# Kernel tuning notes

Measured on AMD Instinct MI355X. Metric: run time of the kernel, lower is better.

The kernel has to match this reference:

```python
import jax, jax.numpy as jnp
import numpy as np

N_NODES = 50000
N_EDGES = 800000
DIM = 64
BN_EPS = 1e-5


def setup_inputs() -> dict:
    key = jax.random.key(0)
    ks = jax.random.split(key, 9)
    s = 1.0 / np.sqrt(DIM)
    feature = jax.random.normal(ks[0], (N_NODES, DIM), jnp.float32)
    edge_index = jax.random.randint(ks[1], (2, N_EDGES), 0, N_NODES)
    Wk = jax.random.normal(ks[2], (DIM, DIM), jnp.float32) * s
    Wq = jax.random.normal(ks[3], (DIM, DIM), jnp.float32) * s
    Wv = jax.random.normal(ks[4], (DIM, DIM), jnp.float32) * s
    bk = jax.random.normal(ks[5], (DIM,), jnp.float32) * 0.01
    bq = jax.random.normal(ks[6], (DIM,), jnp.float32) * 0.01
    bv = jax.random.normal(ks[7], (DIM,), jnp.float32) * 0.01
    bias = jax.random.normal(ks[8], (DIM,), jnp.float32) * 0.01
    gamma = jnp.ones((DIM,), jnp.float32)
    beta = jnp.zeros((DIM,), jnp.float32)
    return dict(feature=feature, edge_index=edge_index, Wk=Wk, bk=bk,
                Wq=Wq, bq=bq, Wv=Wv, bv=bv, bias=bias, gamma=gamma, beta=beta)


def reference(feature, edge_index, Wk, bk, Wq, bq, Wv, bv, bias, gamma, beta):
    # Node-level projections (dense GEMMs on [N, D])
    K = feature @ Wk + bk   # applied to x_i (dst)
    Q = feature @ Wq + bq   # applied to x_j (src)
    V = feature @ Wv + bv   # applied to x_j (src)
    src, dst = edge_index[0], edge_index[1]
    # Per-edge gather -> sigmoid gate -> gated message  [E, D]
    eta = jax.nn.sigmoid(K[dst] + Q[src])
    msg = eta * V[src]
    # Scatter-add into destination nodes  [N, D]
    agg = jax.ops.segment_sum(msg, dst, num_segments=feature.shape[0])
    h = agg + bias
    # BatchNorm1d over nodes (batch statistics, biased variance) + ReLU
    mean = jnp.mean(h, axis=0)
    var = jnp.var(h, axis=0)
    h = (h - mean) * jax.lax.rsqrt(var + BN_EPS) * gamma + beta
    return jax.nn.relu(h)
```

## Files before the change

### kernel.cpp

```cpp
#include <hip/hip_runtime.h>
#include <hip/hip_fp16.h>
#include <stdint.h>

#define N_NODES 50000
#define N_EDGES 800000
#define DIM 64
#define BN_EPS 1e-5f
#define CAP 64
#define ZERO_NODE N_NODES
#define POISON 0xAAAAAAAAu

#define NPTILES 391
#define FUSED_BLOCKS 1173

#define NBINS 241
#define BIN_W 208
#define BINCAP 4352

#define NTILES 3125
#define NSTATS_REP 8

typedef _Float16 f16;
typedef __attribute__((ext_vector_type(8))) _Float16 f16x8;
typedef __attribute__((ext_vector_type(4))) float f32x4;

#define LPITCH 72

__global__ __launch_bounds__(256, 4) void proj_bin_kernel(
    const float* __restrict__ feat,
    const float* __restrict__ Wk, const float* __restrict__ Wq,
    const float* __restrict__ Wv,
    const float* __restrict__ bk, const float* __restrict__ bq,
    const float* __restrict__ bv,
    __half* __restrict__ Kh, __half* __restrict__ QV,
    const int* __restrict__ ei, uint32_t* __restrict__ binCursor,
    uint32_t* __restrict__ binArr)
{
  __shared__ f16 sWt[DIM][LPITCH];
  __shared__ uint32_t hist[NBINS];
  __shared__ uint32_t gbase[NBINS];

  const int b = blockIdx.x;
  const int tid = threadIdx.x;
  const int m3 = b % 3;

  if (m3 != 0) {
    const int sid = (b / 3) * 2 + (m3 - 1);
    const int e0 = sid * 1024;
    const int e1 = (e0 + 1024 < N_EDGES) ? e0 + 1024 : N_EDGES;
    if (tid < NBINS) hist[tid] = 0;
    __syncthreads();

    int n = 0; int bn[4]; uint32_t pk[4], rk[4];
    const int base = e0 + tid * 4;
    if (base + 4 <= e1) {
      const int4 s4 = *(const int4*)(ei + base);
      const int4 d4 = *(const int4*)(ei + N_EDGES + base);
      const int ss[4] = {s4.x, s4.y, s4.z, s4.w};
      const int dd[4] = {d4.x, d4.y, d4.z, d4.w};
#pragma unroll
      for (int j = 0; j < 4; ++j) {
        const int bin = dd[j] / BIN_W;
        bn[j] = bin;
        pk[j] = (uint32_t)ss[j] | ((uint32_t)(dd[j] - bin * BIN_W) << 16);
        rk[j] = atomicAdd(&hist[bin], 1u);
      }
      n = 4;
    } else {
      for (int e = base; e < e1; ++e) {
        const int src = ei[e];
        const int dst = ei[N_EDGES + e];
        const int bin = dst / BIN_W;
        bn[n] = bin;
        pk[n] = (uint32_t)src | ((uint32_t)(dst - bin * BIN_W) << 16);
        rk[n] = atomicAdd(&hist[bin], 1u);
        ++n;
      }
    }
    __syncthreads();
    if (tid < NBINS)
      gbase[tid] = hist[tid] ? (atomicAdd(&binCursor[tid * 16], hist[tid])
                                - POISON) : 0u;
    __syncthreads();
    for (int j = 0; j < n; ++j) {
      const uint32_t pos = gbase[bn[j]] + rk[j];
      if (pos < BINCAP) binArr[(uint32_t)bn[j] * BINCAP + pos] = pk[j];
    }
    return;
  }

  const int tile0 = (b / 3) * 128;
  const int lane = tid & 63;
  const int w = tid >> 6;
  const int nl = lane & 15;
  const int kg = lane >> 4;

  f16x8 fb[2][2];
#pragma unroll
  for (int g2 = 0; g2 < 2; ++g2) {
    const int node = tile0 + w * 32 + g2 * 16 + nl;
    const bool ok = node < N_NODES;
    const float* fp = feat + (size_t)(ok ? node : 0) * DIM;
#pragma unroll
    for (int kk = 0; kk < 2; ++kk) {
      const float4 x0 = ((const float4*)(fp + kk * 32 + kg * 8))[0];
      const float4 x1 = ((const float4*)(fp + kk * 32 + kg * 8))[1];
      f16x8 r;
      r[0] = (f16)x0.x; r[1] = (f16)x0.y; r[2] = (f16)x0.z; r[3] = (f16)x0.w;
      r[4] = (f16)x1.x; r[5] = (f16)x1.y; r[6] = (f16)x1.z; r[7] = (f16)x1.w;
      if (!ok) r = (f16x8)(f16)0.f;
      fb[g2][kk] = r;
    }
  }

#pragma unroll
  for (int m = 0; m < 3; ++m) {
    const float* __restrict__ Wm = (m == 0) ? Wk : (m == 1) ? Wq : Wv;
    const float* __restrict__ bb = (m == 0) ? bk : (m == 1) ? bq : bv;

    __syncthreads();
    for (int i = tid; i < 1024; i += 256) {
      const int c = i & 63;
      const int kq = i >> 6;
      union { f16 h[4]; uint2 u; } pkw;
      pkw.h[0] = (f16)Wm[(kq * 4 + 0) * 64 + c];
      pkw.h[1] = (f16)Wm[(kq * 4 + 1) * 64 + c];
      pkw.h[2] = (f16)Wm[(kq * 4 + 2) * 64 + c];
      pkw.h[3] = (f16)Wm[(kq * 4 + 3) * 64 + c];
      *(uint2*)&sWt[c][kq * 4] = pkw.u;
    }
    __syncthreads();

    f16x8 fa[4][2];
#pragma unroll
    for (int nt = 0; nt < 4; ++nt)
#pragma unroll
      for (int kk = 0; kk < 2; ++kk)
        fa[nt][kk] = *(const f16x8*)&sWt[nt * 16 + nl][kk * 32 + kg * 8];
    f32x4 bias[4];
#pragma unroll
    for (int nt = 0; nt < 4; ++nt)
      bias[nt] = *(const f32x4*)&bb[nt * 16 + kg * 4];

#pragma unroll
    for (int g2 = 0; g2 < 2; ++g2) {
      const int node = tile0 + w * 32 + g2 * 16 + nl;
      f32x4 acc[4];
#pragma unroll
      for (int nt = 0; nt < 4; ++nt) acc[nt] = bias[nt];
#pragma unroll
      for (int kk = 0; kk < 2; ++kk)
#pragma unroll
        for (int nt = 0; nt < 4; ++nt)
          acc[nt] = __builtin_amdgcn_mfma_f32_16x16x32_f16(
              fa[nt][kk], fb[g2][kk], acc[nt], 0, 0, 0);

      if (m == 0) {
        if (node < N_NODES) {
#pragma unroll
          for (int nt = 0; nt < 4; ++nt) {
            union { __half2 h[2]; uint2 u; } pkk;
            pkk.h[0] = __floats2half2_rn(acc[nt][0], acc[nt][1]);
            pkk.h[1] = __floats2half2_rn(acc[nt][2], acc[nt][3]);
            ((uint2*)Kh)[node * 16 + nt * 4 + kg] = pkk.u;
          }
        }
      } else {
        if (node <= N_NODES) {
          const int half = (m == 1) ? 0 : 1;
#pragma unroll
          for (int nt = 0; nt < 4; ++nt) {
            union { __half2 h[2]; uint2 u; } pkk;
            pkk.h[0] = __floats2half2_rn(acc[nt][0], acc[nt][1]);
            pkk.h[1] = __floats2half2_rn(acc[nt][2], acc[nt][3]);
            if (node == N_NODES) { pkk.u.x = 0u; pkk.u.y = 0u; }
            ((uint2*)QV)[node * 32 + (nt * 4 + kg) * 2 + half] = pkk.u;
          }
        }
      }
    }
  }
}

__device__ __forceinline__ float4 edge_acc(float4 acc, const float4 k,
                                           const uint4 qv)
{
  union { uint32_t u; __half2 h; } q0, q1, v0, v1;
  q0.u = qv.x; q1.u = qv.y; v0.u = qv.z; v1.u = qv.w;
  const float2 qa = __half22float2(q0.h);
  const float2 qb = __half22float2(q1.h);
  const float2 va = __half22float2(v0.h);
  const float2 vb = __half22float2(v1.h);
  acc.x += va.x * __builtin_amdgcn_rcpf(1.0f + __expf(-(k.x + qa.x)));
  acc.y += va.y * __builtin_amdgcn_rcpf(1.0f + __expf(-(k.y + qa.y)));
  acc.z += vb.x * __builtin_amdgcn_rcpf(1.0f + __expf(-(k.z + qb.x)));
  acc.w += vb.y * __builtin_amdgcn_rcpf(1.0f + __expf(-(k.w + qb.y)));
  return acc;
}

__global__ __launch_bounds__(256) void aggregate_kernel(
    const uint32_t* __restrict__ binArr, const uint32_t* __restrict__ binCursor,
    const uint2* __restrict__ Kh2, const uint4* __restrict__ QV4,
    float4* __restrict__ agg4, float* __restrict__ stats)
{
  __shared__ uint16_t slist[16][CAP];
  __shared__ uint32_t lcnt[16];
  const int tid = threadIdx.x;
  const int tile = blockIdx.x;
  const int g = tile / 13;
  const uint32_t lo = (uint32_t)((tile - g * 13) * 16);

  if (tid < 16) lcnt[tid] = 0;
  __syncthreads();

  uint32_t cnt = binCursor[g * 16] - POISON;
  if (cnt > BINCAP) cnt = BINCAP;
  const uint32_t* arr = binArr + (uint32_t)g * BINCAP;

  for (uint32_t i = tid * 4; i < cnt; i += 1024) {
    if (i + 4 <= cnt) {
      const uint4 p4 = *(const uint4*)(arr + i);
      const uint32_t ps[4] = {p4.x, p4.y, p4.z, p4.w};
#pragma unroll
      for (int j = 0; j < 4; ++j) {
        const uint32_t idx = (ps[j] >> 16) - lo;
        if (idx < 16u) {
          const uint32_t r = atomicAdd(&lcnt[idx], 1u);
          if (r < CAP) slist[idx][r] = (uint16_t)(ps[j] & 0xFFFFu);
        }
      }
    } else {
      for (uint32_t e = i; e < cnt; ++e) {
        const uint32_t p = arr[e];
        const uint32_t idx = (p >> 16) - lo;
        if (idx < 16u) {
          const uint32_t r = atomicAdd(&lcnt[idx], 1u);
          if (r < CAP) slist[idx][r] = (uint16_t)(p & 0xFFFFu);
        }
      }
    }
  }
  __syncthreads();

  const int row = tid >> 4;
  const int t = tid & 15;
  const int n = tile * 16 + row;

  union { uint2 u; __half2 h[2]; } kun;
  kun.u = Kh2[n * 16 + t];
  const float2 k0 = __half22float2(kun.h[0]);
  const float2 k1 = __half22float2(kun.h[1]);
  const float4 k = make_float4(k0.x, k0.y, k1.x, k1.y);

  int deg = (int)lcnt[row];
  if (deg > CAP) deg = CAP;
  float4 acc = make_float4(0.f, 0.f, 0.f, 0.f);

  for (int j0 = 0; j0 < deg; j0 += 16) {
    const int navail = deg - j0;
    const int s = (t < navail) ? (int)slist[row][j0 + t] : ZERO_NODE;

    int sA[8]; uint4 qvA[8];
#pragma unroll
    for (int i = 0; i < 8; ++i) sA[i] = __shfl(s, i, 16);
#pragma unroll
    for (int i = 0; i < 8; ++i) qvA[i] = QV4[sA[i] * 16 + t];

    const bool haveB = navail > 8;
    int sB[8]; uint4 qvB[8];
    if (haveB) {
#pragma unroll
      for (int i = 0; i < 8; ++i) sB[i] = __shfl(s, 8 + i, 16);
#pragma unroll
      for (int i = 0; i < 8; ++i) qvB[i] = QV4[sB[i] * 16 + t];
    }

#pragma unroll
    for (int i = 0; i < 8; ++i) acc = edge_acc(acc, k, qvA[i]);
    if (haveB) {
#pragma unroll
      for (int i = 0; i < 8; ++i) acc = edge_acc(acc, k, qvB[i]);
    }
  }
  agg4[n * 16 + t] = acc;

  __shared__ float sred[2][16][DIM + 4];
  float4 pssq;
  pssq.x = acc.x * acc.x; pssq.y = acc.y * acc.y;
  pssq.z = acc.z * acc.z; pssq.w = acc.w * acc.w;
  *(float4*)&sred[0][row][t * 4] = acc;
  *(float4*)&sred[1][row][t * 4] = pssq;
  __syncthreads();
  if (tid < 128) {
    const int s = tid >> 6, c = tid & 63;
    float v = 0.0f;
#pragma unroll
    for (int r = 0; r < 16; ++r) v += sred[s][r][c];
    atomicAdd(&stats[(blockIdx.x & (NSTATS_REP - 1)) * 128 + tid], v);
  }
}

__global__ __launch_bounds__(256) void out_kernel(
    float* __restrict__ out, const float* __restrict__ stats,
    const float* __restrict__ gamma, const float* __restrict__ beta)
{
  __shared__ float sstats[128];
  const int tid = threadIdx.x;
  if (tid < 128) {
    float v = 0.0f;
#pragma unroll
    for (int r = 0; r < NSTATS_REP; ++r) v += stats[r * 128 + tid];
    sstats[tid] = v;
  }
  __syncthreads();

  const int idx = blockIdx.x * 256 + tid;
  if (idx >= N_NODES * (DIM / 4)) return;
  const int t = idx & 15;
  const float4 v = ((const float4*)out)[idx];
  const float invN = 1.0f / (float)N_NODES;
  const float vin[4] = { v.x, v.y, v.z, v.w };
  float o[4];
#pragma unroll
  for (int j = 0; j < 4; ++j) {
    const int c = t * 4 + j;
    const float mean = sstats[c] * invN;
    float var = sstats[DIM + c] * invN - mean * mean;
    var = var < 0.0f ? 0.0f : var;
    const float scale = rsqrtf(var + BN_EPS) * gamma[c];
    const float shift = beta[c] - mean * scale;
    const float x = vin[j] * scale + shift;
    o[j] = x > 0.0f ? x : 0.0f;
  }
  float4 r; r.x = o[0]; r.y = o[1]; r.z = o[2]; r.w = o[3];
  ((float4*)out)[idx] = r;
}

extern "C" void kernel_launch(void* const* d_in, const int* in_sizes, int n_in,
                              void* d_out, int out_size, void* d_ws, size_t ws_size,
                              hipStream_t stream) {
  (void)in_sizes; (void)n_in; (void)out_size; (void)ws_size;
  const float* feat  = (const float*)d_in[0];
  const int*   ei    = (const int*)d_in[1];
  const float* Wk    = (const float*)d_in[2];
  const float* bk    = (const float*)d_in[3];
  const float* Wq    = (const float*)d_in[4];
  const float* bq    = (const float*)d_in[5];
  const float* Wv    = (const float*)d_in[6];
  const float* bv    = (const float*)d_in[7];
  const float* gamma = (const float*)d_in[9];
  const float* beta  = (const float*)d_in[10];

  char* base = (char*)d_ws;
  __half*   Kh       = (__half*)base;
  __half*   QV       = (__half*)(base + 6400000);
  float*    stats    = (float*)(base + 19200256);
  uint32_t* binCursor= (uint32_t*)(base + 19204352);
  uint32_t* binArr   = (uint32_t*)(base + 19219776);

  proj_bin_kernel<<<FUSED_BLOCKS, 256, 0, stream>>>(
      feat, Wk, Wq, Wv, bk, bq, bv, Kh, QV, ei, binCursor, binArr);

  aggregate_kernel<<<NTILES, 256, 0, stream>>>(
      binArr, binCursor, (const uint2*)Kh, (const uint4*)QV, (float4*)d_out,
      stats);

  out_kernel<<<(N_NODES * (DIM / 4) + 255) / 256, 256, 0, stream>>>(
      (float*)d_out, stats, gamma, beta);
}
```

Before: 160.3 us.

## Process two 16-node tiles per aggregate block with XCD-aware block remapping

```diff
diff --git a/kernel.cpp b/kernel.cpp
--- a/kernel.cpp
+++ b/kernel.cpp
@@ -13,11 +13,12 @@
 #define NPTILES 391
 #define FUSED_BLOCKS 1173
 
-#define NBINS 241
-#define BIN_W 208
-#define BINCAP 4352
+#define NBINS 224
+#define BIN_W 224
+#define BINCAP 4608
 
 #define NTILES 3125
+#define AGG_BLOCKS 1563
 #define NSTATS_REP 8
 
 typedef _Float16 f16;
@@ -203,14 +204,19 @@
     const uint2* __restrict__ Kh2, const uint4* __restrict__ QV4,
     float4* __restrict__ agg4, float* __restrict__ stats)
 {
-  __shared__ uint16_t slist[16][CAP];
-  __shared__ uint32_t lcnt[16];
+  __shared__ uint16_t slist[32][CAP];
+  __shared__ uint32_t lcnt[32];
   const int tid = threadIdx.x;
-  const int tile = blockIdx.x;
-  const int g = tile / 13;
-  const uint32_t lo = (uint32_t)((tile - g * 13) * 16);
-
-  if (tid < 16) lcnt[tid] = 0;
+
+  const int bid = blockIdx.x;
+  const int xcd = bid % 8;
+  const int start = (xcd < 3) ? xcd * 196 : 3 * 196 + (xcd - 3) * 195;
+  const int w = start + bid / 8;
+
+  const int g = w / 7;
+  const uint32_t lo = (uint32_t)((w - g * 7) * 32);
+
+  if (tid < 32) lcnt[tid] = 0;
   __syncthreads();
 
   uint32_t cnt = binCursor[g * 16] - POISON;
@@ -224,7 +230,7 @@
 #pragma unroll
       for (int j = 0; j < 4; ++j) {
         const uint32_t idx = (ps[j] >> 16) - lo;
-        if (idx < 16u) {
+        if (idx < 32u) {
           const uint32_t r = atomicAdd(&lcnt[idx], 1u);
           if (r < CAP) slist[idx][r] = (uint16_t)(ps[j] & 0xFFFFu);
         }
@@ -233,7 +239,7 @@
       for (uint32_t e = i; e < cnt; ++e) {
         const uint32_t p = arr[e];
         const uint32_t idx = (p >> 16) - lo;
-        if (idx < 16u) {
+        if (idx < 32u) {
           const uint32_t r = atomicAdd(&lcnt[idx], 1u);
           if (r < CAP) slist[idx][r] = (uint16_t)(p & 0xFFFFu);
         }
@@ -244,51 +250,60 @@
 
   const int row = tid >> 4;
   const int t = tid & 15;
-  const int n = tile * 16 + row;
-
-  union { uint2 u; __half2 h[2]; } kun;
-  kun.u = Kh2[n * 16 + t];
-  const float2 k0 = __half22float2(kun.h[0]);
-  const float2 k1 = __half22float2(kun.h[1]);
-  const float4 k = make_float4(k0.x, k0.y, k1.x, k1.y);
-
-  int deg = (int)lcnt[row];
-  if (deg > CAP) deg = CAP;
-  float4 acc = make_float4(0.f, 0.f, 0.f, 0.f);
-
-  for (int j0 = 0; j0 < deg; j0 += 16) {
-    const int navail = deg - j0;
-    const int s = (t < navail) ? (int)slist[row][j0 + t] : ZERO_NODE;
-
-    int sA[8]; uint4 qvA[8];
-#pragma unroll
-    for (int i = 0; i < 8; ++i) sA[i] = __shfl(s, i, 16);
-#pragma unroll
-    for (int i = 0; i < 8; ++i) qvA[i] = QV4[sA[i] * 16 + t];
-
-    const bool haveB = navail > 8;
-    int sB[8]; uint4 qvB[8];
-    if (haveB) {
-#pragma unroll
-      for (int i = 0; i < 8; ++i) sB[i] = __shfl(s, 8 + i, 16);
-#pragma unroll
-      for (int i = 0; i < 8; ++i) qvB[i] = QV4[sB[i] * 16 + t];
-    }
-
-#pragma unroll
-    for (int i = 0; i < 8; ++i) acc = edge_acc(acc, k, qvA[i]);
-    if (haveB) {
-#pragma unroll
-      for (int i = 0; i < 8; ++i) acc = edge_acc(acc, k, qvB[i]);
-    }
-  }
-  agg4[n * 16 + t] = acc;
+  float4 psum = make_float4(0.f, 0.f, 0.f, 0.f);
+  float4 pssq = make_float4(0.f, 0.f, 0.f, 0.f);
+
+#pragma unroll
+  for (int pass = 0; pass < 2; ++pass) {
+    const int tile = w * 2 + pass;
+    if (tile >= NTILES) break;
+    const int lrow = pass * 16 + row;
+    const int n = tile * 16 + row;
+
+    union { uint2 u; __half2 h[2]; } kun;
+    kun.u = Kh2[n * 16 + t];
+    const float2 k0 = __half22float2(kun.h[0]);
+    const float2 k1 = __half22float2(kun.h[1]);
+    const float4 k = make_float4(k0.x, k0.y, k1.x, k1.y);
+
+    int deg = (int)lcnt[lrow];
+    if (deg > CAP) deg = CAP;
+    float4 acc = make_float4(0.f, 0.f, 0.f, 0.f);
+
+    for (int j0 = 0; j0 < deg; j0 += 16) {
+      const int navail = deg - j0;
+      const int s = (t < navail) ? (int)slist[lrow][j0 + t] : ZERO_NODE;
+
+      int sA[8]; uint4 qvA[8];
+#pragma unroll
+      for (int i = 0; i < 8; ++i) sA[i] = __shfl(s, i, 16);
+#pragma unroll
+      for (int i = 0; i < 8; ++i) qvA[i] = QV4[sA[i] * 16 + t];
+
+      const bool haveB = navail > 8;
+      int sB[8]; uint4 qvB[8];
+      if (haveB) {
+#pragma unroll
+        for (int i = 0; i < 8; ++i) sB[i] = __shfl(s, 8 + i, 16);
+#pragma unroll
+        for (int i = 0; i < 8; ++i) qvB[i] = QV4[sB[i] * 16 + t];
+      }
+
+#pragma unroll
+      for (int i = 0; i < 8; ++i) acc = edge_acc(acc, k, qvA[i]);
+      if (haveB) {
+#pragma unroll
+        for (int i = 0; i < 8; ++i) acc = edge_acc(acc, k, qvB[i]);
+      }
+    }
+    agg4[n * 16 + t] = acc;
+    psum.x += acc.x; psum.y += acc.y; psum.z += acc.z; psum.w += acc.w;
+    pssq.x += acc.x * acc.x; pssq.y += acc.y * acc.y;
+    pssq.z += acc.z * acc.z; pssq.w += acc.w * acc.w;
+  }
 
   __shared__ float sred[2][16][DIM + 4];
-  float4 pssq;
-  pssq.x = acc.x * acc.x; pssq.y = acc.y * acc.y;
-  pssq.z = acc.z * acc.z; pssq.w = acc.w * acc.w;
-  *(float4*)&sred[0][row][t * 4] = acc;
+  *(float4*)&sred[0][row][t * 4] = psum;
   *(float4*)&sred[1][row][t * 4] = pssq;
   __syncthreads();
   if (tid < 128) {
@@ -296,7 +311,7 @@
     float v = 0.0f;
 #pragma unroll
     for (int r = 0; r < 16; ++r) v += sred[s][r][c];
-    atomicAdd(&stats[(blockIdx.x & (NSTATS_REP - 1)) * 128 + tid], v);
+    atomicAdd(&stats[(bid & (NSTATS_REP - 1)) * 128 + tid], v);
   }
 }
 
@@ -356,12 +371,12 @@
   __half*   QV       = (__half*)(base + 6400000);
   float*    stats    = (float*)(base + 19200256);
   uint32_t* binCursor= (uint32_t*)(base + 19204352);
-  uint32_t* binArr   = (uint32_t*)(base + 19219776);
+  uint32_t* binArr   = (uint32_t*)(base + 19218688);
 
   proj_bin_kernel<<<FUSED_BLOCKS, 256, 0, stream>>>(
       feat, Wk, Wq, Wv, bk, bq, bv, Kh, QV, ei, binCursor, binArr);
 
-  aggregate_kernel<<<NTILES, 256, 0, stream>>>(
+  aggregate_kernel<<<AGG_BLOCKS, 256, 0, stream>>>(
       binArr, binCursor, (const uint2*)Kh, (const uint4*)QV, (float4*)d_out,
       stats);
 
```

After: 153.3 us (median of 2 runs). 4.4% less time.

## Remap aggregate tiles per XCD, widen bins, preload all weights once

Applied to the files above, without the earlier changes.

```diff
diff --git a/kernel.cpp b/kernel.cpp
--- a/kernel.cpp
+++ b/kernel.cpp
@@ -13,9 +13,9 @@
 #define NPTILES 391
 #define FUSED_BLOCKS 1173
 
-#define NBINS 241
-#define BIN_W 208
-#define BINCAP 4352
+#define NBINS 224
+#define BIN_W 224
+#define BINCAP 4608
 
 #define NTILES 3125
 #define NSTATS_REP 8
@@ -36,7 +36,7 @@
     const int* __restrict__ ei, uint32_t* __restrict__ binCursor,
     uint32_t* __restrict__ binArr)
 {
-  __shared__ f16 sWt[DIM][LPITCH];
+  __shared__ f16 sWt[3][DIM][LPITCH];
   __shared__ uint32_t hist[NBINS];
   __shared__ uint32_t gbase[NBINS];
 
@@ -95,6 +95,20 @@
   const int nl = lane & 15;
   const int kg = lane >> 4;
 
+  for (int i = tid; i < 3 * 1024; i += 256) {
+    const int m = i >> 10;
+    const int rem = i & 1023;
+    const int c = rem & 63;
+    const int kq = rem >> 6;
+    const float* __restrict__ W = (m == 0) ? Wk : (m == 1) ? Wq : Wv;
+    union { f16 h[4]; uint2 u; } pkw;
+    pkw.h[0] = (f16)W[(kq * 4 + 0) * 64 + c];
+    pkw.h[1] = (f16)W[(kq * 4 + 1) * 64 + c];
+    pkw.h[2] = (f16)W[(kq * 4 + 2) * 64 + c];
+    pkw.h[3] = (f16)W[(kq * 4 + 3) * 64 + c];
+    *(uint2*)&sWt[m][c][kq * 4] = pkw.u;
+  }
+
   f16x8 fb[2][2];
 #pragma unroll
   for (int g2 = 0; g2 < 2; ++g2) {
@@ -112,31 +126,18 @@
       fb[g2][kk] = r;
     }
   }
+  __syncthreads();
 
 #pragma unroll
   for (int m = 0; m < 3; ++m) {
-    const float* __restrict__ Wm = (m == 0) ? Wk : (m == 1) ? Wq : Wv;
     const float* __restrict__ bb = (m == 0) ? bk : (m == 1) ? bq : bv;
 
-    __syncthreads();
-    for (int i = tid; i < 1024; i += 256) {
-      const int c = i & 63;
-      const int kq = i >> 6;
-      union { f16 h[4]; uint2 u; } pkw;
-      pkw.h[0] = (f16)Wm[(kq * 4 + 0) * 64 + c];
-      pkw.h[1] = (f16)Wm[(kq * 4 + 1) * 64 + c];
-      pkw.h[2] = (f16)Wm[(kq * 4 + 2) * 64 + c];
-      pkw.h[3] = (f16)Wm[(kq * 4 + 3) * 64 + c];
-      *(uint2*)&sWt[c][kq * 4] = pkw.u;
-    }
-    __syncthreads();
-
     f16x8 fa[4][2];
 #pragma unroll
     for (int nt = 0; nt < 4; ++nt)
 #pragma unroll
       for (int kk = 0; kk < 2; ++kk)
-        fa[nt][kk] = *(const f16x8*)&sWt[nt * 16 + nl][kk * 32 + kg * 8];
+        fa[nt][kk] = *(const f16x8*)&sWt[m][nt * 16 + nl][kk * 32 + kg * 8];
     f32x4 bias[4];
 #pragma unroll
     for (int nt = 0; nt < 4; ++nt)
@@ -206,9 +207,14 @@
   __shared__ uint16_t slist[16][CAP];
   __shared__ uint32_t lcnt[16];
   const int tid = threadIdx.x;
-  const int tile = blockIdx.x;
-  const int g = tile / 13;
-  const uint32_t lo = (uint32_t)((tile - g * 13) * 16);
+
+  const int bid = blockIdx.x;
+  const int xcd = bid % 8;
+  const int start = (xcd < 5) ? xcd * 391 : 5 * 391 + (xcd - 5) * 390;
+  const int w = start + bid / 8;
+
+  const int g = w / 14;
+  const uint32_t lo = (uint32_t)((w - g * 14) * 16);
 
   if (tid < 16) lcnt[tid] = 0;
   __syncthreads();
@@ -244,7 +250,7 @@
 
   const int row = tid >> 4;
   const int t = tid & 15;
-  const int n = tile * 16 + row;
+  const int n = w * 16 + row;
 
   union { uint2 u; __half2 h[2]; } kun;
   kun.u = Kh2[n * 16 + t];
@@ -296,7 +302,7 @@
     float v = 0.0f;
 #pragma unroll
     for (int r = 0; r < 16; ++r) v += sred[s][r][c];
-    atomicAdd(&stats[(blockIdx.x & (NSTATS_REP - 1)) * 128 + tid], v);
+    atomicAdd(&stats[(bid & (NSTATS_REP - 1)) * 128 + tid], v);
   }
 }
 
@@ -356,7 +362,7 @@
   __half*   QV       = (__half*)(base + 6400000);
   float*    stats    = (float*)(base + 19200256);
   uint32_t* binCursor= (uint32_t*)(base + 19204352);
-  uint32_t* binArr   = (uint32_t*)(base + 19219776);
+  uint32_t* binArr   = (uint32_t*)(base + 19218688);
 
   proj_bin_kernel<<<FUSED_BLOCKS, 256, 0, stream>>>(
       feat, Wk, Wq, Wv, bk, bq, bv, Kh, QV, ei, binCursor, binArr);
```

New measurement: 157.5 us. About the same (-1.8%).
